# Kernel tuning notes

Hardware: AMD Instinct MI355X
Metric: run time of the kernel (lower is better)

The kernel has to match this reference:

```python
import jax, jax.numpy as jnp
import numpy as np

G, N, E, F, C, H = 2, 20000, 160000, 128, 64, 8
NEG_SLOPE = 0.2


def setup_inputs() -> dict:
    key = jax.random.key(0)
    ks = jax.random.split(key, 16)
    def w(k, shape, fan_in):
        return jax.random.normal(k, shape, jnp.float32) * (1.0 / np.sqrt(fan_in))
    z = lambda *s: jnp.zeros(s, jnp.float32)
    return {
        "x": jax.random.normal(ks[0], (G, N, F), jnp.float32),
        "edge_index": jax.random.randint(ks[1], (G, 2, E), 0, N, jnp.int32),
        "edge_weight": jax.random.uniform(ks[2], (G, E), jnp.float32),
        "Wl1": w(ks[3], (F, H * C), F), "bl1": z(H * C),
        "Wr1": w(ks[4], (F, H * C), F), "br1": z(H * C),
        "We1": w(ks[5], (1, H * C), 1),
        "att1": w(ks[6], (H, C), C),
        "bias1": z(H * C),
        "Wl2": w(ks[7], (H * C, C), H * C), "bl2": z(C),
        "Wr2": w(ks[8], (H * C, C), H * C), "br2": z(C),
        "We2": w(ks[9], (1, C), 1),
        "att2": w(ks[10], (1, C), C),
        "bias2": z(C),
        "Wg": w(ks[11], (C, C), C), "bg": z(C),
        "Wn": w(ks[12], (2 * C, C), 2 * C), "bn": z(C),
        "Wo": w(ks[13], (C, 1), C), "bo": z(1),
    }


def _segment_softmax(logits, seg, n):
    m = jax.ops.segment_max(logits, seg, num_segments=n)
    ex = jnp.exp(logits - m[seg])
    den = jax.ops.segment_sum(ex, seg, num_segments=n)
    return ex / den[seg]


def _gatv2(x, src, dst, eattr, Wl, bl, Wr, br, We, att, bias, heads, concat):
    # Faithful PyG GATv2Conv (share_weights=False, edge_dim=1).
    n = x.shape[0]
    hc = Wl.shape[1]
    c = hc // heads
    xl = (x @ Wl + bl).reshape(n, heads, c)   # lin_l (source / message)
    xr = (x @ Wr + br).reshape(n, heads, c)   # lin_r (target)
    ee = (eattr @ We).reshape(-1, heads, c)   # lin_edge (bias=False)
    s = jax.nn.leaky_relu(xl[src] + xr[dst] + ee, NEG_SLOPE)  # [Etot, H, C]
    logit = jnp.einsum('ehc,hc->eh', s, att)
    alpha = _segment_softmax(logit, dst, n)   # softmax over incoming edges
    out = jax.ops.segment_sum(alpha[..., None] * xl[src], dst, num_segments=n)
    out = out.reshape(n, hc) if concat else out.mean(axis=1)
    return out + bias


def _forward(edge_index, x, edge_weight, Wl1, bl1, Wr1, br1, We1, att1, bias1,
             Wl2, bl2, Wr2, br2, We2, att2, bias2, Wg, bg, Wn, bn, Wo, bo):
    n = x.shape[1]
    def per_graph(xg, eig, ewg):
        src, dst = eig[0], eig[1]
        ea = ewg[:, None]  # edge_weight.unsqueeze(-1), edge_dim=1
        # add_self_loops with fill_value='mean' (mean of edge_attr grouped by dst)
        cnt = jax.ops.segment_sum(jnp.ones_like(ewg), dst, num_segments=n)
        loop = jax.ops.segment_sum(ea, dst, num_segments=n) / jnp.clip(cnt, 1.0)[:, None]
        ar = jnp.arange(n, dtype=src.dtype)
        src2 = jnp.concatenate([src, ar])
        dst2 = jnp.concatenate([dst, ar])
        ea2 = jnp.concatenate([ea, loop], axis=0)
        h = jax.nn.elu(_gatv2(xg, src2, dst2, ea2, Wl1, bl1, Wr1, br1, We1, att1, bias1, H, True))
        h = jax.nn.elu(_gatv2(h, src2, dst2, ea2, Wl2, bl2, Wr2, br2, We2, att2, bias2, 1, False))
        return h
    h = jax.vmap(per_graph)(x, edge_index, edge_weight)      # [G, N, C]
    g_emb = h.max(axis=1)                                    # global_max_pool per graph
    Gv = g_emb.max(axis=0)                                   # max over graphs -> [C]
    Gv = jax.nn.relu(Gv @ Wg + bg)
    Hc = jnp.concatenate([h, jnp.broadcast_to(Gv, h.shape)], axis=-1)  # [G,N,2C]
    h2 = jax.nn.relu(Hc @ Wn + bn)
    return (h2 @ Wo + bo)[..., 0]                            # [G, N] logits


def reference(x, edge_index, edge_weight, Wl1, bl1, Wr1, br1, We1, att1, bias1,
              Wl2, bl2, Wr2, br2, We2, att2, bias2, Wg, bg, Wn, bn, Wo, bo):
    return _forward(edge_index, x, edge_weight, Wl1, bl1, Wr1, br1, We1, att1, bias1,
                    Wl2, bl2, Wr2, br2, We2, att2, bias2, Wg, bg, Wn, bn, Wo, bo)
```

## Files before the change

kernel.cpp:

```cpp
#include <hip/hip_runtime.h>
#include <hip/hip_bf16.h>
#include <cstdint>
#include <cstddef>

#define NEG_SLOPE 0.2f

static constexpr int Gg = 2;
static constexpr int Nn = 20000;
static constexpr int Ee = 160000;
static constexpr int Ff = 128;
static constexpr int Cc = 64;
static constexpr int HC = 512;
static constexpr int GN = Gg * Nn;
static constexpr int GNP = 40064;
static constexpr int DEGMAX = 48;

typedef __attribute__((ext_vector_type(8))) short short8;
typedef __attribute__((ext_vector_type(4))) float floatx4;

__device__ __forceinline__ float bf2f(unsigned short b) {
    return __uint_as_float(((unsigned)b) << 16);
}
__device__ __forceinline__ unsigned short f2bf(float x) {
    unsigned u = __float_as_uint(x);
    unsigned r = 0x7fffu + ((u >> 16) & 1u);
    return (unsigned short)((u + r) >> 16);
}
__device__ __forceinline__ void unpack8(const uint4 p, float* f) {
    f[0] = __uint_as_float(p.x << 16); f[1] = __uint_as_float(p.x & 0xffff0000u);
    f[2] = __uint_as_float(p.y << 16); f[3] = __uint_as_float(p.y & 0xffff0000u);
    f[4] = __uint_as_float(p.z << 16); f[5] = __uint_as_float(p.z & 0xffff0000u);
    f[6] = __uint_as_float(p.w << 16); f[7] = __uint_as_float(p.w & 0xffff0000u);
}
__device__ __forceinline__ void unpack4(const uint2 p, float* f) {
    f[0] = __uint_as_float(p.x << 16); f[1] = __uint_as_float(p.x & 0xffff0000u);
    f[2] = __uint_as_float(p.y << 16); f[3] = __uint_as_float(p.y & 0xffff0000u);
}
__device__ __forceinline__ unsigned encf(float x) {
    unsigned u = __float_as_uint(x);
    return (u & 0x80000000u) ? ~u : (u | 0x80000000u);
}
__device__ __forceinline__ float decf(unsigned e) {
    return __uint_as_float((e & 0x80000000u) ? (e ^ 0x80000000u) : ~e);
}

__global__ void castprep_k(const float* __restrict__ x, unsigned short* __restrict__ xb,
                           const float* __restrict__ Wl1, const float* __restrict__ Wr1,
                           const float* __restrict__ bl1, const float* __restrict__ br1,
                           const float* __restrict__ Wl2, const float* __restrict__ Wr2,
                           const float* __restrict__ bl2, const float* __restrict__ br2,
                           unsigned short* __restrict__ Wt1, unsigned short* __restrict__ Wt2,
                           float* __restrict__ b1cat, float* __restrict__ b2cat,
                           int* __restrict__ cnt, unsigned* __restrict__ gmax) {
    int t = blockIdx.x * 256 + threadIdx.x;
    size_t base = (size_t)t * 4;
    if (base < (size_t)GNP * Ff) {
        ushort4 ov;
        if (base < (size_t)GN * Ff) {
            float4 v = *(const float4*)(x + base);
            ov.x = f2bf(v.x); ov.y = f2bf(v.y); ov.z = f2bf(v.z); ov.w = f2bf(v.w);
        } else {
            ov.x = ov.y = ov.z = ov.w = 0;
        }
        *(ushort4*)(xb + base) = ov;
    }
    if (t < 1024 * 128) {
        int n = t >> 7, k = t & 127;
        float v = (n < 512) ? Wl1[(size_t)k * 512 + n] : Wr1[(size_t)k * 512 + n - 512];
        Wt1[t] = f2bf(v);
    }
    if (t < 128 * 512) {
        int n = t >> 9, k = t & 511;
        float v = (n < 64) ? Wl2[(size_t)k * 64 + n] : Wr2[(size_t)k * 64 + n - 64];
        Wt2[t] = f2bf(v);
    }
    if (t < 1024) b1cat[t] = (t < 512) ? bl1[t] : br1[t - 512];
    if (t < 128)  b2cat[t] = (t < 64) ? bl2[t] : br2[t - 64];
    if (t < GN)   cnt[t] = 0;
    if (t < 1024) gmax[t] = 0u;
}

template <int K, bool EDGES>
__global__ __launch_bounds__(256) void mfma_gemm_k(const unsigned short* __restrict__ A, int lda,
                                                   const unsigned short* __restrict__ Bt,
                                                   const float* __restrict__ bias,
                                                   unsigned short* __restrict__ Cg, int ldc,
                                                   int Mreal,
                                                   const int* __restrict__ ei,
                                                   const float* __restrict__ ew,
                                                   int* __restrict__ cnt,
                                                   int2* __restrict__ sedge) {
    if (EDGES) {
        int bid = blockIdx.y * gridDim.x + blockIdx.x;
        int idx = bid * 256 + threadIdx.x;
        if (idx < Gg * Ee) {
            int g = (idx >= Ee) ? 1 : 0;
            int e = idx - g * Ee;
            int src = ei[(size_t)g * 2 * Ee + e];
            int dst = ei[(size_t)g * 2 * Ee + Ee + e];
            float wv = ew[idx];
            int node = g * Nn + dst;
            int pos = atomicAdd(&cnt[node], 1);
            if (pos < DEGMAX) {
                int2 v; v.x = src; v.y = __float_as_int(wv);
                sedge[(size_t)node * DEGMAX + pos] = v;
            }
        }
    }

    __shared__ unsigned short As[128 * 32];
    __shared__ unsigned short Bs[128 * 32];
    const int t = threadIdx.x;
    const int lane = t & 63;
    const int wid = t >> 6;
    const int wm = wid >> 1, wn = wid & 1;
    const int m0 = blockIdx.x * 128;
    const int n0 = blockIdx.y * 128;

    floatx4 acc[4][4] = {};

    const int jrow = t >> 2;
    const int js = t & 3;
    const int wavebase = (t & 192) * 16;

    for (int k0 = 0; k0 < K; k0 += 32) {
#pragma unroll
        for (int r = 0; r < 2; ++r) {
            int row = jrow + r * 64;
            int c = js ^ ((row >> 1) & 3);
            const unsigned short* gA = A + (size_t)(m0 + row) * lda + k0 + c * 8;
            const unsigned short* gB = Bt + (size_t)(n0 + row) * K + k0 + c * 8;
            __builtin_amdgcn_global_load_lds(
                (const __attribute__((address_space(1))) void*)gA,
                (__attribute__((address_space(3))) void*)((char*)As + r * 4096 + wavebase),
                16, 0, 0);
            __builtin_amdgcn_global_load_lds(
                (const __attribute__((address_space(1))) void*)gB,
                (__attribute__((address_space(3))) void*)((char*)Bs + r * 4096 + wavebase),
                16, 0, 0);
        }
        __syncthreads();

        const int lrow = lane & 15, lc = lane >> 4;
        short8 af[4], bf[4];
#pragma unroll
        for (int i2 = 0; i2 < 4; ++i2) {
            int rA = wm * 64 + i2 * 16 + lrow;
            int sA = lc ^ ((rA >> 1) & 3);
            af[i2] = *(const short8*)((const char*)As + (rA * 4 + sA) * 16);
        }
#pragma unroll
        for (int j2 = 0; j2 < 4; ++j2) {
            int rB = wn * 64 + j2 * 16 + lrow;
            int sB = lc ^ ((rB >> 1) & 3);
            bf[j2] = *(const short8*)((const char*)Bs + (rB * 4 + sB) * 16);
        }
#pragma unroll
        for (int i2 = 0; i2 < 4; ++i2)
#pragma unroll
            for (int j2 = 0; j2 < 4; ++j2)
                acc[i2][j2] = __builtin_amdgcn_mfma_f32_16x16x32_bf16(bf[j2], af[i2], acc[i2][j2], 0, 0, 0);
        __syncthreads();
    }

    const int mrow = m0 + wm * 64 + (lane & 15);
    const int ncol0 = n0 + wn * 64 + ((lane >> 4) << 2);
    float4 bq[4];
#pragma unroll
    for (int j2 = 0; j2 < 4; ++j2) bq[j2] = *(const float4*)(bias + ncol0 + j2 * 16);
#pragma unroll
    for (int i2 = 0; i2 < 4; ++i2) {
        int m = mrow + i2 * 16;
        if (m < Mreal) {
#pragma unroll
            for (int j2 = 0; j2 < 4; ++j2) {
                ushort4 ov;
                ov.x = f2bf(acc[i2][j2][0] + bq[j2].x);
                ov.y = f2bf(acc[i2][j2][1] + bq[j2].y);
                ov.z = f2bf(acc[i2][j2][2] + bq[j2].z);
                ov.w = f2bf(acc[i2][j2][3] + bq[j2].w);
                *(ushort4*)(Cg + (size_t)m * ldc + ncol0 + j2 * 16) = ov;
            }
        }
    }
}

__global__ __launch_bounds__(128) void gemm2_k(const unsigned short* __restrict__ A, int lda,
                                               const unsigned short* __restrict__ Bt,
                                               const float* __restrict__ bias,
                                               unsigned short* __restrict__ Cg,
                                               int Mreal) {
    __shared__ unsigned short As[64 * 32];
    __shared__ unsigned short Bs[128 * 32];
    const int t = threadIdx.x;
    const int lane = t & 63;
    const int wn = t >> 6;
    const int m0 = blockIdx.x * 64;

    floatx4 acc[4][4] = {};
    const int wavebase = (t & 64) * 16;

    for (int k0 = 0; k0 < HC; k0 += 32) {
#pragma unroll
        for (int it = 0; it < 2; ++it) {
            int slot = t + it * 128;
            int row = slot >> 2;
            int c = (slot & 3) ^ ((row >> 1) & 3);
            const unsigned short* gA = A + (size_t)(m0 + row) * lda + k0 + c * 8;
            __builtin_amdgcn_global_load_lds(
                (const __attribute__((address_space(1))) void*)gA,
                (__attribute__((address_space(3))) void*)((char*)As + it * 2048 + wavebase),
                16, 0, 0);
        }
#pragma unroll
        for (int it = 0; it < 4; ++it) {
            int slot = t + it * 128;
            int row = slot >> 2;
            int c = (slot & 3) ^ ((row >> 1) & 3);
            const unsigned short* gB = Bt + (size_t)row * HC + k0 + c * 8;
            __builtin_amdgcn_global_load_lds(
                (const __attribute__((address_space(1))) void*)gB,
                (__attribute__((address_space(3))) void*)((char*)Bs + it * 2048 + wavebase),
                16, 0, 0);
        }
        __syncthreads();

        const int lrow = lane & 15, lc = lane >> 4;
        short8 af[4], bf[4];
#pragma unroll
        for (int i2 = 0; i2 < 4; ++i2) {
            int rA = i2 * 16 + lrow;
            int sA = lc ^ ((rA >> 1) & 3);
            af[i2] = *(const short8*)((const char*)As + (rA * 4 + sA) * 16);
        }
#pragma unroll
        for (int j2 = 0; j2 < 4; ++j2) {
            int rB = wn * 64 + j2 * 16 + lrow;
            int sB = lc ^ ((rB >> 1) & 3);
            bf[j2] = *(const short8*)((const char*)Bs + (rB * 4 + sB) * 16);
        }
#pragma unroll
        for (int i2 = 0; i2 < 4; ++i2)
#pragma unroll
            for (int j2 = 0; j2 < 4; ++j2)
                acc[i2][j2] = __builtin_amdgcn_mfma_f32_16x16x32_bf16(bf[j2], af[i2], acc[i2][j2], 0, 0, 0);
        __syncthreads();
    }

    const int mrow = m0 + (lane & 15);
    const int ncol0 = wn * 64 + ((lane >> 4) << 2);
    float4 bq[4];
#pragma unroll
    for (int j2 = 0; j2 < 4; ++j2) bq[j2] = *(const float4*)(bias + ncol0 + j2 * 16);
#pragma unroll
    for (int i2 = 0; i2 < 4; ++i2) {
        int m = mrow + i2 * 16;
        if (m < Mreal) {
#pragma unroll
            for (int j2 = 0; j2 < 4; ++j2) {
                ushort4 ov;
                ov.x = f2bf(acc[i2][j2][0] + bq[j2].x);
                ov.y = f2bf(acc[i2][j2][1] + bq[j2].y);
                ov.z = f2bf(acc[i2][j2][2] + bq[j2].z);
                ov.w = f2bf(acc[i2][j2][3] + bq[j2].w);
                *(ushort4*)(Cg + (size_t)m * 128 + ncol0 + j2 * 16) = ov;
            }
        }
    }
}

__global__ __launch_bounds__(256) void agg1_k(const unsigned short* xlr,
                                              const int2* __restrict__ sedge,
                                              const int* __restrict__ cnt,
                                              const float* __restrict__ att1, const float* __restrict__ We1,
                                              const float* __restrict__ bias1,
                                              unsigned short* h1, float* __restrict__ loopw,
                                              int nbase) {
    const int lane = threadIdx.x & 63;
    const int node = nbase + (blockIdx.x << 2) + (threadIdx.x >> 6);
    const int g = (node >= Nn) ? 1 : 0;

    float attv[8], wev[8];
    {
        float4 a0 = *(const float4*)(att1 + lane * 8);
        float4 a1 = *(const float4*)(att1 + lane * 8 + 4);
        attv[0] = a0.x; attv[1] = a0.y; attv[2] = a0.z; attv[3] = a0.w;
        attv[4] = a1.x; attv[5] = a1.y; attv[6] = a1.z; attv[7] = a1.w;
        float4 w0 = *(const float4*)(We1 + lane * 8);
        float4 w1 = *(const float4*)(We1 + lane * 8 + 4);
        wev[0] = w0.x; wev[1] = w0.y; wev[2] = w0.z; wev[3] = w0.w;
        wev[4] = w1.x; wev[5] = w1.y; wev[6] = w1.z; wev[7] = w1.w;
    }
    float xrv[8];
    unpack8(((const uint4*)(xlr + (size_t)node * 1024 + 512))[lane], xrv);

    const int ec = cnt[node];
    const int2* ep = sedge + (size_t)node * DEGMAX;
    const uint4* rowb = (const uint4*)(xlr + (size_t)g * Nn * 1024) + lane;

    float lsum = 0.f, wsum = 0.f;
    float acc[8] = {};

    uint4 r0, r1; int2 s0v, s1v;
    if (ec > 0) { s0v = ep[0]; r0 = rowb[(size_t)s0v.x * 128]; }
    if (ec > 1) { s1v = ep[1]; r1 = rowb[(size_t)s1v.x * 128]; }
    int e = 0;
    while (e + 1 < ec) {
        uint4 r2, r3; int2 s2v, s3v;
        if (e + 2 < ec) { s2v = ep[e + 2]; r2 = rowb[(size_t)s2v.x * 128]; }
        if (e + 3 < ec) { s3v = ep[e + 3]; r3 = rowb[(size_t)s3v.x * 128]; }
        float xa[8], xb_[8];
        unpack8(r0, xa);
        unpack8(r1, xb_);
        float wa = __int_as_float(s0v.y), wb = __int_as_float(s1v.y);
        wsum += wa + wb;
        float ta = 0.f, tb = 0.f;
#pragma unroll
        for (int j = 0; j < 8; ++j) {
            float sa = xa[j] + fmaf(wa, wev[j], xrv[j]);
            float sb = xb_[j] + fmaf(wb, wev[j], xrv[j]);
            sa = fmaxf(sa, NEG_SLOPE * sa);
            sb = fmaxf(sb, NEG_SLOPE * sb);
            ta = fmaf(sa, attv[j], ta);
            tb = fmaf(sb, attv[j], tb);
        }
        ta += __shfl_xor(ta, 1); tb += __shfl_xor(tb, 1);
        ta += __shfl_xor(ta, 2); tb += __shfl_xor(tb, 2);
        ta += __shfl_xor(ta, 4); tb += __shfl_xor(tb, 4);
        float pa = __expf(ta), pb = __expf(tb);
        lsum += pa + pb;
#pragma unroll
        for (int j = 0; j < 8; ++j) acc[j] = fmaf(pa, xa[j], fmaf(pb, xb_[j], acc[j]));
        r0 = r2; s0v = s2v; r1 = r3; s1v = s3v;
        e += 2;
    }
    if (e < ec) {
        float xa[8];
        unpack8(r0, xa);
        float wa = __int_as_float(s0v.y);
        wsum += wa;
        float ta = 0.f;
#pragma unroll
        for (int j = 0; j < 8; ++j) {
            float sa = xa[j] + fmaf(wa, wev[j], xrv[j]);
            sa = fmaxf(sa, NEG_SLOPE * sa);
            ta = fmaf(sa, attv[j], ta);
        }
        ta += __shfl_xor(ta, 1); ta += __shfl_xor(ta, 2); ta += __shfl_xor(ta, 4);
        float pa = __expf(ta);
        lsum += pa;
#pragma unroll
        for (int j = 0; j < 8; ++j) acc[j] = fmaf(pa, xa[j], acc[j]);
    }

    float lw = wsum / fmaxf((float)ec, 1.f);
    {
        float xv[8];
        unpack8(((const uint4*)(xlr + (size_t)node * 1024))[lane], xv);
        float tp = 0.f;
#pragma unroll
        for (int j = 0; j < 8; ++j) {
            float s = xv[j] + fmaf(lw, wev[j], xrv[j]);
            s = fmaxf(s, NEG_SLOPE * s);
            tp = fmaf(s, attv[j], tp);
        }
        tp += __shfl_xor(tp, 1); tp += __shfl_xor(tp, 2); tp += __shfl_xor(tp, 4);
        float p = __expf(tp);
        lsum += p;
#pragma unroll
        for (int j = 0; j < 8; ++j) acc[j] = fmaf(p, xv[j], acc[j]);
    }

    float inv = 1.f / lsum;
    float4 b0 = *(const float4*)(bias1 + lane * 8);
    float4 b1 = *(const float4*)(bias1 + lane * 8 + 4);
    float bvv[8] = {b0.x, b0.y, b0.z, b0.w, b1.x, b1.y, b1.z, b1.w};
    float ov[8];
#pragma unroll
    for (int j = 0; j < 8; ++j) {
        float o = fmaf(acc[j], inv, bvv[j]);
        ov[j] = o > 0.f ? o : (__expf(o) - 1.f);
    }
    uint4 pk;
    pk.x = (unsigned)f2bf(ov[0]) | ((unsigned)f2bf(ov[1]) << 16);
    pk.y = (unsigned)f2bf(ov[2]) | ((unsigned)f2bf(ov[3]) << 16);
    pk.z = (unsigned)f2bf(ov[4]) | ((unsigned)f2bf(ov[5]) << 16);
    pk.w = (unsigned)f2bf(ov[6]) | ((unsigned)f2bf(ov[7]) << 16);
    ((uint4*)(h1 + (size_t)node * 1024))[lane] = pk;
    if (lane == 0) loopw[node] = lw;
}

__global__ __launch_bounds__(1024) void agg2_k(const unsigned short* __restrict__ xlr2,
                                               const int2* __restrict__ sedge,
                                               const int* __restrict__ cnt,
                                               const float* __restrict__ loopw,
                                               const float* __restrict__ att2, const float* __restrict__ We2,
                                               const float* __restrict__ bias2,
                                               float* __restrict__ hout, unsigned* __restrict__ gmax) {
    const int tid = threadIdx.x;
    const int lane = tid & 63;
    const int cs = lane & 15;
    const int sub = lane >> 4;
    const int node = blockIdx.x * 16 + (tid >> 6);
    const int g = (node >= Nn) ? 1 : 0;

    float4 av = *(const float4*)(att2 + cs * 4);
    float4 wv4 = *(const float4*)(We2 + cs * 4);
    float attv[4] = {av.x, av.y, av.z, av.w};
    float wevv[4] = {wv4.x, wv4.y, wv4.z, wv4.w};
    float xrv[4];
    unpack4(*(const uint2*)(xlr2 + (size_t)node * 128 + 64 + cs * 4), xrv);
    const unsigned short* rowb = xlr2 + (size_t)g * Nn * 128;

    const int ec = cnt[node];
    const int2* ep = sedge + (size_t)node * DEGMAX;
    const int lo = (ec * sub) >> 2;
    const int hi = (ec * (sub + 1)) >> 2;

    float lsum = 0.f, acc[4] = {};

    int e = lo;
    uint2 r0 = {0, 0}, r1 = {0, 0};
    int2 s0v = {0, 0}, s1v = {0, 0};
    if (e < hi)     { s0v = ep[e];     r0 = *(const uint2*)(rowb + (size_t)s0v.x * 128 + cs * 4); }
    if (e + 1 < hi) { s1v = ep[e + 1]; r1 = *(const uint2*)(rowb + (size_t)s1v.x * 128 + cs * 4); }
    while (e + 1 < hi) {
        uint2 r2 = {0, 0}, r3 = {0, 0};
        int2 s2v = {0, 0}, s3v = {0, 0};
        if (e + 2 < hi) { s2v = ep[e + 2]; r2 = *(const uint2*)(rowb + (size_t)s2v.x * 128 + cs * 4); }
        if (e + 3 < hi) { s3v = ep[e + 3]; r3 = *(const uint2*)(rowb + (size_t)s3v.x * 128 + cs * 4); }
        float xa[4], xb_[4];
        unpack4(r0, xa);
        unpack4(r1, xb_);
        float wa = __int_as_float(s0v.y), wb = __int_as_float(s1v.y);
        float ta = 0.f, tb = 0.f;
#pragma unroll
        for (int j = 0; j < 4; ++j) {
            float sa = xa[j] + fmaf(wa, wevv[j], xrv[j]);
            float sb = xb_[j] + fmaf(wb, wevv[j], xrv[j]);
            sa = fmaxf(sa, NEG_SLOPE * sa);
            sb = fmaxf(sb, NEG_SLOPE * sb);
            ta = fmaf(sa, attv[j], ta);
            tb = fmaf(sb, attv[j], tb);
        }
        ta += __shfl_xor(ta, 1); tb += __shfl_xor(tb, 1);
        ta += __shfl_xor(ta, 2); tb += __shfl_xor(tb, 2);
        ta += __shfl_xor(ta, 4); tb += __shfl_xor(tb, 4);
        ta += __shfl_xor(ta, 8); tb += __shfl_xor(tb, 8);
        float pa = __expf(ta), pb = __expf(tb);
        lsum += pa + pb;
#pragma unroll
        for (int j = 0; j < 4; ++j) acc[j] = fmaf(pa, xa[j], fmaf(pb, xb_[j], acc[j]));
        r0 = r2; s0v = s2v; r1 = r3; s1v = s3v;
        e += 2;
    }
    if (e < hi) {
        float xa[4];
        unpack4(r0, xa);
        float wa = __int_as_float(s0v.y);
        float ta = 0.f;
#pragma unroll
        for (int j = 0; j < 4; ++j) {
            float sa = xa[j] + fmaf(wa, wevv[j], xrv[j]);
            sa = fmaxf(sa, NEG_SLOPE * sa);
            ta = fmaf(sa, attv[j], ta);
        }
        ta += __shfl_xor(ta, 1); ta += __shfl_xor(ta, 2);
        ta += __shfl_xor(ta, 4); ta += __shfl_xor(ta, 8);
        float pa = __expf(ta);
        lsum += pa;
#pragma unroll
        for (int j = 0; j < 4; ++j) acc[j] = fmaf(pa, xa[j], acc[j]);
    }

    lsum += __shfl_xor(lsum, 16); lsum += __shfl_xor(lsum, 32);
#pragma unroll
    for (int j = 0; j < 4; ++j) {
        acc[j] += __shfl_xor(acc[j], 16);
        acc[j] += __shfl_xor(acc[j], 32);
    }

    {
        float lw = loopw[node];
        float xv[4];
        unpack4(*(const uint2*)(xlr2 + (size_t)node * 128 + cs * 4), xv);
        float tp = 0.f;
#pragma unroll
        for (int j = 0; j < 4; ++j) {
            float s = xv[j] + fmaf(lw, wevv[j], xrv[j]);
            s = fmaxf(s, NEG_SLOPE * s);
            tp = fmaf(s, attv[j], tp);
        }
        tp += __shfl_xor(tp, 1); tp += __shfl_xor(tp, 2);
        tp += __shfl_xor(tp, 4); tp += __shfl_xor(tp, 8);
        float p = __expf(tp);
        lsum += p;
#pragma unroll
        for (int j = 0; j < 4; ++j) acc[j] = fmaf(p, xv[j], acc[j]);
    }

    float inv = 1.f / lsum;
    float4 bv = *(const float4*)(bias2 + cs * 4);
    float bvv[4] = {bv.x, bv.y, bv.z, bv.w};
    float ov[4];
#pragma unroll
    for (int j = 0; j < 4; ++j) {
        float o = fmaf(acc[j], inv, bvv[j]);
        ov[j] = o > 0.f ? o : (__expf(o) - 1.f);
    }
    if (sub == 0) {
        float4 o4;
        o4.x = ov[0]; o4.y = ov[1]; o4.z = ov[2]; o4.w = ov[3];
        *(float4*)(hout + (size_t)node * Cc + cs * 4) = o4;
    }

    __shared__ unsigned bm[64];
    if (tid < 64) bm[tid] = 0u;
    __syncthreads();
    if (sub == 0) {
#pragma unroll
        for (int j = 0; j < 4; ++j) atomicMax(&bm[cs * 4 + j], encf(ov[j]));
    }
    __syncthreads();
    if (tid < 64) atomicMax(&gmax[tid * 16], bm[tid]);
}

__global__ __launch_bounds__(256) void final_k(const float* __restrict__ h,
                                               const unsigned* __restrict__ gmax,
                                               const float* __restrict__ Wg, const float* __restrict__ bg,
                                               const float* __restrict__ Wn, const float* __restrict__ bn,
                                               const float* __restrict__ Wo, const float* __restrict__ bo,
                                               float* __restrict__ out) {
    __shared__ float wns[64 * 64];
    __shared__ float g0s[64], g1s[64], cvs[64];
    const int tid = threadIdx.x;
    for (int k = tid; k < 64 * 64; k += 256) wns[k] = Wn[k];
    if (tid < 64) g0s[tid] = decf(gmax[tid * 16]);
    __syncthreads();
    if (tid < 64) {
        float a = bg[tid];
        for (int c = 0; c < 64; ++c) a += g0s[c] * Wg[c * 64 + tid];
        g1s[tid] = fmaxf(a, 0.f);
    }
    __syncthreads();
    if (tid < 64) {
        float b = bn[tid];
        for (int c = 0; c < 64; ++c) b += g1s[c] * Wn[(64 + c) * 64 + tid];
        cvs[tid] = b;
    }
    __syncthreads();

    const int lane = tid & 63;
    const int cs = lane & 15;
    const int sub = lane >> 4;
    float4 wo4 = *(const float4*)(Wo + cs * 4);
    float woa[4] = {wo4.x, wo4.y, wo4.z, wo4.w};
    float cv0 = cvs[cs * 4 + 0], cv1 = cvs[cs * 4 + 1], cv2 = cvs[cs * 4 + 2], cv3 = cvs[cs * 4 + 3];
    float bo0 = bo[0];

#pragma unroll
    for (int nb = 0; nb < 4; ++nb) {
        const int node = blockIdx.x * 64 + nb * 16 + (tid >> 6) * 4 + sub;
        float4 h4 = *(const float4*)(h + (size_t)node * Cc + cs * 4);
        float hv[4] = {h4.x, h4.y, h4.z, h4.w};
        float inner[4] = {cv0, cv1, cv2, cv3};
#pragma unroll
        for (int c = 0; c < 64; ++c) {
            float hc = __shfl(hv[c & 3], sub * 16 + (c >> 2));
            float4 wv = *(const float4*)&wns[c * 64 + cs * 4];
            inner[0] = fmaf(hc, wv.x, inner[0]);
            inner[1] = fmaf(hc, wv.y, inner[1]);
            inner[2] = fmaf(hc, wv.z, inner[2]);
            inner[3] = fmaf(hc, wv.w, inner[3]);
        }
        float t = 0.f;
#pragma unroll
        for (int j = 0; j < 4; ++j) {
            float v = fmaxf(inner[j], 0.f);
            t = fmaf(v, woa[j], t);
        }
        t += __shfl_xor(t, 1); t += __shfl_xor(t, 2);
        t += __shfl_xor(t, 4); t += __shfl_xor(t, 8);
        if (cs == 0) out[node] = t + bo0;
    }
}

extern "C" void kernel_launch(void* const* d_in, const int* in_sizes, int n_in,
                              void* d_out, int out_size, void* d_ws, size_t ws_size,
                              hipStream_t stream) {
    const float* x     = (const float*)d_in[0];
    const int*   ei    = (const int*)d_in[1];
    const float* ew    = (const float*)d_in[2];
    const float* Wl1   = (const float*)d_in[3];
    const float* bl1v  = (const float*)d_in[4];
    const float* Wr1   = (const float*)d_in[5];
    const float* br1v  = (const float*)d_in[6];
    const float* We1   = (const float*)d_in[7];
    const float* att1  = (const float*)d_in[8];
    const float* bias1 = (const float*)d_in[9];
    const float* Wl2   = (const float*)d_in[10];
    const float* bl2v  = (const float*)d_in[11];
    const float* Wr2   = (const float*)d_in[12];
    const float* br2v  = (const float*)d_in[13];
    const float* We2   = (const float*)d_in[14];
    const float* att2  = (const float*)d_in[15];
    const float* bias2 = (const float*)d_in[16];
    const float* Wg    = (const float*)d_in[17];
    const float* bgv   = (const float*)d_in[18];
    const float* Wn    = (const float*)d_in[19];
    const float* bnv   = (const float*)d_in[20];
    const float* Wo    = (const float*)d_in[21];
    const float* bov   = (const float*)d_in[22];
    float* out = (float*)d_out;

    char* w = (char*)d_ws;
    size_t o = 0;
    auto take = [&](size_t b) -> char* {
        char* p = w + o;
        o += (b + 255) & ~(size_t)255;
        return p;
    };
    unsigned short* xlr1 = (unsigned short*)take((size_t)GNP * 1024 * 2);
    unsigned short* xb   = (unsigned short*)take((size_t)GNP * Ff * 2);
    unsigned short* xlr2 = (unsigned short*)take((size_t)GNP * 128 * 2);
    unsigned short* Wt1  = (unsigned short*)take(1024 * 128 * 2);
    unsigned short* Wt2  = (unsigned short*)take(128 * 512 * 2);
    float* b1cat = (float*)take(1024 * 4);
    float* b2cat = (float*)take(128 * 4);
    int*    cnt   = (int*)take((size_t)GN * 4);
    float*  loopw = (float*)take((size_t)GN * 4);
    int2*   sedge = (int2*)take((size_t)GN * DEGMAX * 8);
    unsigned* gmax = (unsigned*)take(1024 * 4);
    unsigned short* h1 = xlr1 + 512;
    float* hbuf = (float*)xb;

    castprep_k<<<((GNP * Ff / 4) + 255) / 256, 256, 0, stream>>>(
        x, xb, Wl1, Wr1, bl1v, br1v, Wl2, Wr2, bl2v, br2v, Wt1, Wt2, b1cat, b2cat, cnt, gmax);

    mfma_gemm_k<Ff, true><<<dim3(GNP / 128, 8), 256, 0, stream>>>(
        xb, Ff, Wt1, b1cat, xlr1, 1024, GN, ei, ew, cnt, sedge);

    agg1_k<<<GN / 8, 256, 0, stream>>>(xlr1, sedge, cnt, att1, We1, bias1, h1, loopw, 0);
    agg1_k<<<GN / 8, 256, 0, stream>>>(xlr1, sedge, cnt, att1, We1, bias1, h1, loopw, GN / 2);

    gemm2_k<<<GNP / 64, 128, 0, stream>>>(h1, 1024, Wt2, b2cat, xlr2, GN);

    agg2_k<<<GN / 16, 1024, 0, stream>>>(xlr2, sedge, cnt, loopw, att2, We2, bias2, hbuf, gmax);

    final_k<<<GN / 64, 256, 0, stream>>>(hbuf, gmax, Wg, bgv, Wn, bnv, Wo, bov, out);

    (void)in_sizes; (void)n_in; (void)out_size; (void)ws_size;
}
```

Before: 339.8 us.

## Load full-K tiles once in gemm1, move edge bucketing to prep, merge agg1 launches

The first-layer GEMM now stages the entire K=128 A and B tiles into LDS in a single pass with a 16-way XOR swizzle, dropping the per-k-step barriers. Edge bucketing into per-node lists moves from the GEMM kernel into the cast/prep kernel, and the count array is zeroed with a memset beforehand. The two half-size agg1 launches become one. The cost is 64 KB of LDS per block, which may reduce occupancy, and the GEMM can no longer overlap the atomic scatter.

After: 330.2 us, median of 2. -2.8%, faster.

```diff
diff --git a/kernel.cpp b/kernel.cpp
--- a/kernel.cpp
+++ b/kernel.cpp
@@ -51,7 +51,9 @@
                            const float* __restrict__ bl2, const float* __restrict__ br2,
                            unsigned short* __restrict__ Wt1, unsigned short* __restrict__ Wt2,
                            float* __restrict__ b1cat, float* __restrict__ b2cat,
-                           int* __restrict__ cnt, unsigned* __restrict__ gmax) {
+                           int* __restrict__ cnt, unsigned* __restrict__ gmax,
+                           const int* __restrict__ ei, const float* __restrict__ ew,
+                           int2* __restrict__ sedge) {
     int t = blockIdx.x * 256 + threadIdx.x;
     size_t base = (size_t)t * 4;
     if (base < (size_t)GNP * Ff) {
@@ -76,40 +78,29 @@
     }
     if (t < 1024) b1cat[t] = (t < 512) ? bl1[t] : br1[t - 512];
     if (t < 128)  b2cat[t] = (t < 64) ? bl2[t] : br2[t - 64];
-    if (t < GN)   cnt[t] = 0;
     if (t < 1024) gmax[t] = 0u;
-}
-
-template <int K, bool EDGES>
-__global__ __launch_bounds__(256) void mfma_gemm_k(const unsigned short* __restrict__ A, int lda,
-                                                   const unsigned short* __restrict__ Bt,
-                                                   const float* __restrict__ bias,
-                                                   unsigned short* __restrict__ Cg, int ldc,
-                                                   int Mreal,
-                                                   const int* __restrict__ ei,
-                                                   const float* __restrict__ ew,
-                                                   int* __restrict__ cnt,
-                                                   int2* __restrict__ sedge) {
-    if (EDGES) {
-        int bid = blockIdx.y * gridDim.x + blockIdx.x;
-        int idx = bid * 256 + threadIdx.x;
-        if (idx < Gg * Ee) {
-            int g = (idx >= Ee) ? 1 : 0;
-            int e = idx - g * Ee;
-            int src = ei[(size_t)g * 2 * Ee + e];
-            int dst = ei[(size_t)g * 2 * Ee + Ee + e];
-            float wv = ew[idx];
-            int node = g * Nn + dst;
-            int pos = atomicAdd(&cnt[node], 1);
-            if (pos < DEGMAX) {
-                int2 v; v.x = src; v.y = __float_as_int(wv);
-                sedge[(size_t)node * DEGMAX + pos] = v;
-            }
-        }
-    }
-
-    __shared__ unsigned short As[128 * 32];
-    __shared__ unsigned short Bs[128 * 32];
+    if (t < Gg * Ee) {
+        int g = (t >= Ee) ? 1 : 0;
+        int e = t - g * Ee;
+        int src = ei[(size_t)g * 2 * Ee + e];
+        int dst = ei[(size_t)g * 2 * Ee + Ee + e];
+        float wv = ew[t];
+        int node = g * Nn + dst;
+        int pos = atomicAdd(&cnt[node], 1);
+        if (pos < DEGMAX) {
+            int2 v; v.x = src; v.y = __float_as_int(wv);
+            sedge[(size_t)node * DEGMAX + pos] = v;
+        }
+    }
+}
+
+__global__ __launch_bounds__(256) void gemm1_k(const unsigned short* __restrict__ A,
+                                               const unsigned short* __restrict__ Bt,
+                                               const float* __restrict__ bias,
+                                               unsigned short* __restrict__ Cg,
+                                               int Mreal) {
+    __shared__ unsigned short As[128 * 128];
+    __shared__ unsigned short Bs[128 * 128];
     const int t = threadIdx.x;
     const int lane = t & 63;
     const int wid = t >> 6;
@@ -117,54 +108,52 @@
     const int m0 = blockIdx.x * 128;
     const int n0 = blockIdx.y * 128;
 
+#pragma unroll
+    for (int it = 0; it < 8; ++it) {
+        int slin = t + it * 256;
+        int row = slin >> 4;
+        int sc = slin & 15;
+        int c = sc ^ (row & 15);
+        const unsigned short* gA = A + (size_t)(m0 + row) * Ff + c * 8;
+        const unsigned short* gB = Bt + (size_t)(n0 + row) * Ff + c * 8;
+        int ldsbase = (it * 256 + (t & 192)) * 16;
+        __builtin_amdgcn_global_load_lds(
+            (const __attribute__((address_space(1))) void*)gA,
+            (__attribute__((address_space(3))) void*)((char*)As + ldsbase),
+            16, 0, 0);
+        __builtin_amdgcn_global_load_lds(
+            (const __attribute__((address_space(1))) void*)gB,
+            (__attribute__((address_space(3))) void*)((char*)Bs + ldsbase),
+            16, 0, 0);
+    }
+    __syncthreads();
+
     floatx4 acc[4][4] = {};
-
-    const int jrow = t >> 2;
-    const int js = t & 3;
-    const int wavebase = (t & 192) * 16;
-
-    for (int k0 = 0; k0 < K; k0 += 32) {
-#pragma unroll
-        for (int r = 0; r < 2; ++r) {
-            int row = jrow + r * 64;
-            int c = js ^ ((row >> 1) & 3);
-            const unsigned short* gA = A + (size_t)(m0 + row) * lda + k0 + c * 8;
-            const unsigned short* gB = Bt + (size_t)(n0 + row) * K + k0 + c * 8;
-            __builtin_amdgcn_global_load_lds(
-                (const __attribute__((address_space(1))) void*)gA,
-                (__attribute__((address_space(3))) void*)((char*)As + r * 4096 + wavebase),
-                16, 0, 0);
-            __builtin_amdgcn_global_load_lds(
-                (const __attribute__((address_space(1))) void*)gB,
-                (__attribute__((address_space(3))) void*)((char*)Bs + r * 4096 + wavebase),
-                16, 0, 0);
-        }
-        __syncthreads();
-
-        const int lrow = lane & 15, lc = lane >> 4;
+    const int lrow = lane & 15, lc = lane >> 4;
+#pragma unroll
+    for (int k0 = 0; k0 < 4; ++k0) {
         short8 af[4], bf[4];
 #pragma unroll
         for (int i2 = 0; i2 < 4; ++i2) {
             int rA = wm * 64 + i2 * 16 + lrow;
-            int sA = lc ^ ((rA >> 1) & 3);
-            af[i2] = *(const short8*)((const char*)As + (rA * 4 + sA) * 16);
+            int slot = (k0 * 4 + lc) ^ (rA & 15);
+            af[i2] = *(const short8*)((const char*)As + rA * 256 + slot * 16);
         }
 #pragma unroll
         for (int j2 = 0; j2 < 4; ++j2) {
             int rB = wn * 64 + j2 * 16 + lrow;
-            int sB = lc ^ ((rB >> 1) & 3);
-            bf[j2] = *(const short8*)((const char*)Bs + (rB * 4 + sB) * 16);
+            int slot = (k0 * 4 + lc) ^ (rB & 15);
+            bf[j2] = *(const short8*)((const char*)Bs + rB * 256 + slot * 16);
         }
 #pragma unroll
         for (int i2 = 0; i2 < 4; ++i2)
 #pragma unroll
             for (int j2 = 0; j2 < 4; ++j2)
                 acc[i2][j2] = __builtin_amdgcn_mfma_f32_16x16x32_bf16(bf[j2], af[i2], acc[i2][j2], 0, 0, 0);
-        __syncthreads();
-    }
-
-    const int mrow = m0 + wm * 64 + (lane & 15);
-    const int ncol0 = n0 + wn * 64 + ((lane >> 4) << 2);
+    }
+
+    const int mrow = m0 + wm * 64 + lrow;
+    const int ncol0 = n0 + wn * 64 + (lc << 2);
     float4 bq[4];
 #pragma unroll
     for (int j2 = 0; j2 < 4; ++j2) bq[j2] = *(const float4*)(bias + ncol0 + j2 * 16);
@@ -179,7 +168,7 @@
                 ov.y = f2bf(acc[i2][j2][1] + bq[j2].y);
                 ov.z = f2bf(acc[i2][j2][2] + bq[j2].z);
                 ov.w = f2bf(acc[i2][j2][3] + bq[j2].w);
-                *(ushort4*)(Cg + (size_t)m * ldc + ncol0 + j2 * 16) = ov;
+                *(ushort4*)(Cg + (size_t)m * 1024 + ncol0 + j2 * 16) = ov;
             }
         }
     }
@@ -274,10 +263,10 @@
                                               const int* __restrict__ cnt,
                                               const float* __restrict__ att1, const float* __restrict__ We1,
                                               const float* __restrict__ bias1,
-                                              unsigned short* h1, float* __restrict__ loopw,
-                                              int nbase) {
+                                              unsigned short* h1, float* __restrict__ loopw) {
     const int lane = threadIdx.x & 63;
-    const int node = nbase + (blockIdx.x << 2) + (threadIdx.x >> 6);
+    const int node = (blockIdx.x << 2) + (threadIdx.x >> 6);
+    if (node >= GN) return;
     const int g = (node >= Nn) ? 1 : 0;
 
     float attv[8], wev[8];
@@ -634,14 +623,15 @@
     unsigned short* h1 = xlr1 + 512;
     float* hbuf = (float*)xb;
 
+    hipMemsetAsync(cnt, 0, (size_t)GN * 4, stream);
+
     castprep_k<<<((GNP * Ff / 4) + 255) / 256, 256, 0, stream>>>(
-        x, xb, Wl1, Wr1, bl1v, br1v, Wl2, Wr2, bl2v, br2v, Wt1, Wt2, b1cat, b2cat, cnt, gmax);
-
-    mfma_gemm_k<Ff, true><<<dim3(GNP / 128, 8), 256, 0, stream>>>(
-        xb, Ff, Wt1, b1cat, xlr1, 1024, GN, ei, ew, cnt, sedge);
-
-    agg1_k<<<GN / 8, 256, 0, stream>>>(xlr1, sedge, cnt, att1, We1, bias1, h1, loopw, 0);
-    agg1_k<<<GN / 8, 256, 0, stream>>>(xlr1, sedge, cnt, att1, We1, bias1, h1, loopw, GN / 2);
+        x, xb, Wl1, Wr1, bl1v, br1v, Wl2, Wr2, bl2v, br2v, Wt1, Wt2, b1cat, b2cat,
+        cnt, gmax, ei, ew, sedge);
+
+    gemm1_k<<<dim3(GNP / 128, 8), 256, 0, stream>>>(xb, Wt1, b1cat, xlr1, GN);
+
+    agg1_k<<<GN / 4, 256, 0, stream>>>(xlr1, sedge, cnt, att1, We1, bias1, h1, loopw);
 
     gemm2_k<<<GNP / 64, 128, 0, stream>>>(h1, 1024, Wt2, b2cat, xlr2, GN);
 
```
